# Kernel optimization log

Measured on AMD Instinct MI355X. Metric: run time of the kernel, lower is better.

## Reference

```python
import jax, jax.numpy as jnp
import numpy as np

N = 32768      # total points (multiple of patch_size -> no padding needed)
C = 768        # channels
H = 8          # num heads
K = 256        # patch_size (window length)
HD = C // H    # head dim = 96, divisible by 6 (3 axes * rotary pairs)
FREQ = 100.0   # rope_freq


def rope3d(x, pos):
    """Point-position RoPE: head dim split into 3 axis chunks, each rotated
    by angles pos_axis * freq**(-i/half).  x: [N,H,HD], pos: [N,3] float."""
    d_axis = HD // 3            # 32
    half = d_axis // 2          # 16
    inv_freq = FREQ ** (-jnp.arange(half, dtype=x.dtype) / half)   # [half]
    ang = pos[:, :, None] * inv_freq[None, None, :]                # [N,3,half]
    cos = jnp.cos(ang)[:, None, :, :]                              # [N,1,3,half]
    sin = jnp.sin(ang)[:, None, :, :]
    xr = x.reshape(x.shape[0], x.shape[1], 3, d_axis)              # [N,H,3,d_axis]
    x1, x2 = xr[..., :half], xr[..., half:]
    out = jnp.concatenate([x1 * cos - x2 * sin, x1 * sin + x2 * cos], axis=-1)
    return out.reshape(x.shape)


def setup_inputs() -> dict:
    key = jax.random.key(0)
    ks = jax.random.split(key, 6)
    feat = jax.random.normal(ks[0], (N, C), dtype=jnp.float32)
    grid_coord = jax.random.randint(ks[1], (N, 3), 0, 1024, dtype=jnp.int32)
    order = jax.random.permutation(ks[2], N).astype(jnp.int32)     # serialized order
    inverse = jnp.argsort(order).astype(jnp.int32)                 # its inverse
    w_qkv = jax.random.normal(ks[3], (C, 3 * C), dtype=jnp.float32) * 0.02
    b_qkv = jnp.zeros((3 * C,), dtype=jnp.float32)
    w_proj = jax.random.normal(ks[4], (C, C), dtype=jnp.float32) * 0.02
    b_proj = jnp.zeros((C,), dtype=jnp.float32)
    return {"feat": feat, "grid_coord": grid_coord, "order": order,
            "inverse": inverse, "w_qkv": w_qkv, "b_qkv": b_qkv,
            "w_proj": w_proj, "b_proj": b_proj}


def reference(feat, grid_coord, order, inverse, w_qkv, b_qkv, w_proj, b_proj):
    scale = HD ** -0.5
    P = N // K  # number of windows
    qkv = (feat @ w_qkv + b_qkv)[order]                   # gather by serialized order
    pos = grid_coord[order].astype(feat.dtype)            # [N,3]
    q, k, v = jnp.split(qkv, 3, axis=-1)
    q = rope3d(q.reshape(N, H, HD), pos)
    k = rope3d(k.reshape(N, H, HD), pos)
    v = v.reshape(N, H, HD)
    # windowed (varlen with equal patch lengths) attention
    qw = q.reshape(P, K, H, HD)
    kw = k.reshape(P, K, H, HD)
    vw = v.reshape(P, K, H, HD)
    logits = jnp.einsum('pqhd,pkhd->phqk', qw, kw) * scale
    attn = jax.nn.softmax(logits, axis=-1)
    out = jnp.einsum('phqk,pkhd->pqhd', attn, vw).reshape(N, C)
    out = out[inverse]                                    # scatter back to input order
    return out @ w_proj + b_proj
```

## Files before the change

### kernel.cpp

```cpp
#include <hip/hip_runtime.h>
#include <hip/hip_bf16.h>
#include <stdint.h>

typedef __bf16 bf16_t;
typedef __bf16 bf16x8 __attribute__((ext_vector_type(8)));
typedef __bf16 bf16x4 __attribute__((ext_vector_type(4)));
typedef float f32x4 __attribute__((ext_vector_type(4)));

__device__ __forceinline__ void gload_lds16(const bf16_t* g, bf16_t* l) {
  __builtin_amdgcn_global_load_lds((const __attribute__((address_space(1))) void*)g,
                                   (__attribute__((address_space(3))) void*)l, 16, 0, 0);
}

__global__ __launch_bounds__(256) void transpose_cast_k(const float* __restrict__ W,
                                                        bf16_t* __restrict__ Bt,
                                                        int KDin, int MDin) {
  __shared__ float tile[64][65];
  const int bm = blockIdx.x, bk = blockIdx.y;
  const int c = threadIdx.x & 63, r0 = threadIdx.x >> 6;
#pragma unroll
  for (int rr = 0; rr < 16; ++rr) {
    int row = rr * 4 + r0;
    tile[row][c] = W[(size_t)(bk * 64 + row) * MDin + bm * 64 + c];
  }
  __syncthreads();
#pragma unroll
  for (int rr = 0; rr < 16; ++rr) {
    int mo = rr * 4 + r0;
    Bt[(size_t)(bm * 64 + mo) * KDin + bk * 64 + c] = (bf16_t)tile[c][mo];
  }
}

__global__ __launch_bounds__(256) void gather_cast_k(const float* __restrict__ feat,
                                                     const int* __restrict__ order,
                                                     const int* __restrict__ grid_coord,
                                                     bf16_t* __restrict__ featp,
                                                     float* __restrict__ posf) {
  const int id = blockIdx.x * 256 + threadIdx.x;
  const int j = id / 192;
  const int c = (id % 192) * 4;
  const int g = order[j];
  const float4 v = *(const float4*)(feat + (size_t)g * 768 + c);
  bf16x4 o;
  o[0] = (bf16_t)v.x; o[1] = (bf16_t)v.y; o[2] = (bf16_t)v.z; o[3] = (bf16_t)v.w;
  *(bf16x4*)(featp + (size_t)j * 768 + c) = o;
  if (c == 0) {
    posf[j * 3 + 0] = (float)grid_coord[g * 3 + 0];
    posf[j * 3 + 1] = (float)grid_coord[g * 3 + 1];
    posf[j * 3 + 2] = (float)grid_coord[g * 3 + 2];
  }
}

template <int MODE>
__global__ __launch_bounds__(256) void gemm_bt_k(const bf16_t* __restrict__ A,
                                                 const bf16_t* __restrict__ Bt,
                                                 const float* __restrict__ bias,
                                                 bf16_t* __restrict__ Cq,
                                                 bf16_t* __restrict__ Ck,
                                                 bf16_t* __restrict__ Cv,
                                                 float* __restrict__ Cf,
                                                 const int* __restrict__ order,
                                                 const float* __restrict__ posf) {
  __shared__ bf16_t As[128 * 32];
  __shared__ bf16_t Bs[128 * 32];
  const int tid = threadIdx.x;
  const int lane = tid & 63;
  const int wave = tid >> 6;
  const int wr = wave >> 1, wc = wave & 1;
  const int lq = lane & 15, lk = lane >> 4;
  const int bx = blockIdx.x, by = blockIdx.y;

  const bf16_t* gA = A + (size_t)(by * 128 + (tid >> 2)) * 768 + (tid & 3) * 8;
  const bf16_t* gB = Bt + (size_t)(bx * 128 + (tid >> 2)) * 768 + (tid & 3) * 8;
  bf16_t* lA = As + tid * 8;
  bf16_t* lB = Bs + tid * 8;

  f32x4 acc[4][4] = {};

  for (int kk = 0; kk < 24; ++kk) {
    gload_lds16(gA, lA);
    gload_lds16(gA + 64 * 768, lA + 2048);
    gload_lds16(gB, lB);
    gload_lds16(gB + 64 * 768, lB + 2048);
    gA += 32;
    gB += 32;
    __syncthreads();
    bf16x8 af[4], bfr[4];
#pragma unroll
    for (int t = 0; t < 4; ++t) {
      af[t]  = *(const bf16x8*)(As + (wr * 64 + t * 16 + lq) * 32 + lk * 8);
      bfr[t] = *(const bf16x8*)(Bs + (wc * 64 + t * 16 + lq) * 32 + lk * 8);
    }
#pragma unroll
    for (int mt = 0; mt < 4; ++mt)
#pragma unroll
      for (int nt = 0; nt < 4; ++nt)
        acc[mt][nt] = __builtin_amdgcn_mfma_f32_16x16x32_bf16(af[mt], bfr[nt], acc[mt][nt], 0, 0, 0);
    __syncthreads();
  }

  const int colb = bx * 128 + wc * 64;
  float bcol[4];
#pragma unroll
  for (int nt = 0; nt < 4; ++nt) bcol[nt] = bias[colb + nt * 16 + lq];

  if (MODE == 0) {
    bf16_t* base = (bx < 6) ? Cq : (bx < 12 ? Ck : Cv);
    const int coll = colb - (bx < 6 ? 0 : (bx < 12 ? 768 : 1536));
    if (bx < 12) {
      const int a0 = (colb % 96) >> 5;
      const int a1 = ((colb + 32) % 96) >> 5;
      const float fr = exp2f(-0.41524101186f * (float)lq);
#pragma unroll
      for (int mt = 0; mt < 4; ++mt) {
        const int rowb = by * 128 + wr * 64 + mt * 16 + lk * 4;
#pragma unroll
        for (int r = 0; r < 4; ++r) {
          const int row = rowb + r;
          float s0, c0, s1, c1;
          __sincosf(posf[row * 3 + a0] * fr, &s0, &c0);
          __sincosf(posf[row * 3 + a1] * fr, &s1, &c1);
          const float x1 = acc[mt][0][r] + bcol[0], x2 = acc[mt][1][r] + bcol[1];
          const float y1 = acc[mt][2][r] + bcol[2], y2 = acc[mt][3][r] + bcol[3];
          acc[mt][0][r] = x1 * c0 - x2 * s0;
          acc[mt][1][r] = x1 * s0 + x2 * c0;
          acc[mt][2][r] = y1 * c1 - y2 * s1;
          acc[mt][3][r] = y1 * s1 + y2 * c1;
        }
#pragma unroll
        for (int nt = 0; nt < 4; ++nt) {
          const int col = coll + nt * 16 + lq;
#pragma unroll
          for (int r = 0; r < 4; ++r)
            base[(size_t)(rowb + r) * 768 + col] = (bf16_t)acc[mt][nt][r];
        }
      }
    } else {
#pragma unroll
      for (int mt = 0; mt < 4; ++mt) {
        const int rowb = by * 128 + wr * 64 + mt * 16 + lk * 4;
#pragma unroll
        for (int nt = 0; nt < 4; ++nt) {
          const int col = coll + nt * 16 + lq;
#pragma unroll
          for (int r = 0; r < 4; ++r)
            base[(size_t)(rowb + r) * 768 + col] = (bf16_t)(acc[mt][nt][r] + bcol[nt]);
        }
      }
    }
  } else {
#pragma unroll
    for (int mt = 0; mt < 4; ++mt) {
      const int rowb = by * 128 + wr * 64 + mt * 16 + lk * 4;
      int ro[4];
#pragma unroll
      for (int r = 0; r < 4; ++r) ro[r] = order[rowb + r];
#pragma unroll
      for (int nt = 0; nt < 4; ++nt) {
        const int col = colb + nt * 16 + lq;
#pragma unroll
        for (int r = 0; r < 4; ++r)
          Cf[(size_t)ro[r] * 768 + col] = acc[mt][nt][r] + bcol[nt];
      }
    }
  }
}

__global__ __launch_bounds__(256) void pack_k(const bf16_t* __restrict__ Kb,
                                              const bf16_t* __restrict__ Vb,
                                              bf16_t* __restrict__ Kp,
                                              bf16_t* __restrict__ Vp) {
  __shared__ bf16_t VT[96 * 264];
  const int h = blockIdx.x, p = blockIdx.y;
  const int tid = threadIdx.x;
  const int tok0 = p * 256;
  const size_t phb = (size_t)(p * 8 + h) * 24576;

#pragma unroll
  for (int i = 0; i < 12; ++i) {
    const int c = i * 256 + tid;
    const int fi = c >> 6, ln = c & 63;
    const int nt = fi / 3, a = fi - nt * 3;
    const int tok = nt * 16 + (ln & 15), feat = a * 32 + (ln >> 4) * 8;
    *(bf16x8*)(Kp + phb + (size_t)c * 8) =
        *(const bf16x8*)(Kb + (size_t)(tok0 + tok) * 768 + h * 96 + feat);
  }

  {
    const bf16_t* vrow = Vb + (size_t)(tok0 + tid) * 768 + h * 96;
#pragma unroll
    for (int d0 = 0; d0 < 96; d0 += 8) {
      bf16x8 v = *(const bf16x8*)(vrow + d0);
#pragma unroll
      for (int i = 0; i < 8; ++i) VT[(d0 + i) * 264 + tid] = v[i];
    }
  }
  __syncthreads();
#pragma unroll
  for (int i = 0; i < 12; ++i) {
    const int c = i * 256 + tid;
    const int fi = c >> 6, ln = c & 63;
    const int d = (fi >> 3) * 16 + (ln & 15);
    const int tb = (fi & 7) * 32 + (ln >> 4) * 8;
    *(bf16x8*)(Vp + phb + (size_t)c * 8) = *(const bf16x8*)(VT + d * 264 + tb);
  }
}

__global__ __launch_bounds__(256) void attn_k(bf16_t* QO,
                                              const bf16_t* __restrict__ Kp,
                                              const bf16_t* __restrict__ Vp) {
  __shared__ bf16_t KV[24576];
  __shared__ bf16_t Pb[4][2048];
  const int bid = blockIdx.x;
  const int chunk = bid & 3;
  const int ph = bid >> 2;
  const int h = ph & 7, p = ph >> 3;
  const int tid = threadIdx.x, lane = tid & 63, wave = tid >> 6;
  const int lq = lane & 15, lk = lane >> 4;
  const int tok0 = p * 256;
  const int qrow0 = chunk * 64 + wave * 16;
  const bf16_t* Kps = Kp + (size_t)ph * 24576;
  const bf16_t* Vps = Vp + (size_t)ph * 24576;
  const float scale = 0.10206207262f;

#pragma unroll
  for (int i = 0; i < 12; ++i)
    gload_lds16(Kps + i * 2048 + tid * 8, KV + i * 2048 + tid * 8);
  bf16x8 aq[3];
  {
    const bf16_t* qb = QO + (size_t)(tok0 + qrow0 + lq) * 768 + h * 96 + lk * 8;
#pragma unroll
    for (int kc = 0; kc < 3; ++kc) aq[kc] = *(const bf16x8*)(qb + kc * 32);
  }
  __syncthreads();

  f32x4 sacc[16];
#pragma unroll
  for (int nt = 0; nt < 16; ++nt) {
    f32x4 acc = {0.f, 0.f, 0.f, 0.f};
#pragma unroll
    for (int kc = 0; kc < 3; ++kc) {
      bf16x8 bk = *(const bf16x8*)(KV + (size_t)((nt * 3 + kc) * 64 + lane) * 8);
      acc = __builtin_amdgcn_mfma_f32_16x16x32_bf16(aq[kc], bk, acc, 0, 0, 0);
    }
    sacc[nt] = acc;
  }
  __syncthreads();

#pragma unroll
  for (int i = 0; i < 12; ++i)
    gload_lds16(Vps + i * 2048 + tid * 8, KV + i * 2048 + tid * 8);

  float linv[4];
#pragma unroll
  for (int r = 0; r < 4; ++r) {
    float mx = -1e30f;
#pragma unroll
    for (int nt = 0; nt < 16; ++nt) mx = fmaxf(mx, sacc[nt][r]);
    mx = fmaxf(mx, __shfl_xor(mx, 1));
    mx = fmaxf(mx, __shfl_xor(mx, 2));
    mx = fmaxf(mx, __shfl_xor(mx, 4));
    mx = fmaxf(mx, __shfl_xor(mx, 8));
    mx *= scale;
    float l = 0.f;
#pragma unroll
    for (int nt = 0; nt < 16; ++nt) {
      float e = __expf(sacc[nt][r] * scale - mx);
      sacc[nt][r] = e;
      l += e;
    }
    l += __shfl_xor(l, 1);
    l += __shfl_xor(l, 2);
    l += __shfl_xor(l, 4);
    l += __shfl_xor(l, 8);
    linv[r] = 1.f / l;
  }
  __syncthreads();

  bf16_t* pw = &Pb[wave][0];
  f32x4 oacc[6] = {};
#pragma unroll
  for (int hf = 0; hf < 2; ++hf) {
#pragma unroll
    for (int ntl = 0; ntl < 8; ++ntl) {
      const int nt = hf * 8 + ntl;
      const int chk = ntl * 2 + (lq >> 3);
#pragma unroll
      for (int r = 0; r < 4; ++r) {
        const int row = lk * 4 + r;
        const int phys = chk ^ (row & 7);
        pw[row * 128 + phys * 8 + (lq & 7)] = (bf16_t)sacc[nt][r];
      }
    }
#pragma unroll
    for (int kcl = 0; kcl < 4; ++kcl) {
      const int physr = (kcl * 4 + lk) ^ (lq & 7);
      bf16x8 pf = *(const bf16x8*)(pw + lq * 128 + physr * 8);
      const int kc = hf * 4 + kcl;
#pragma unroll
      for (int dt = 0; dt < 6; ++dt) {
        bf16x8 vb = *(const bf16x8*)(KV + (size_t)((dt * 8 + kc) * 64 + lane) * 8);
        oacc[dt] = __builtin_amdgcn_mfma_f32_16x16x32_bf16(pf, vb, oacc[dt], 0, 0, 0);
      }
    }
  }

#pragma unroll
  for (int dt = 0; dt < 6; ++dt) {
#pragma unroll
    for (int r = 0; r < 4; ++r) {
      const int row = tok0 + qrow0 + lk * 4 + r;
      QO[(size_t)row * 768 + h * 96 + dt * 16 + lq] = (bf16_t)(oacc[dt][r] * linv[r]);
    }
  }
}

extern "C" void kernel_launch(void* const* d_in, const int* in_sizes, int n_in,
                              void* d_out, int out_size, void* d_ws, size_t ws_size,
                              hipStream_t stream) {
  const float* feat       = (const float*)d_in[0];
  const int*   grid_coord = (const int*)d_in[1];
  const int*   order      = (const int*)d_in[2];
  const float* w_qkv      = (const float*)d_in[4];
  const float* b_qkv      = (const float*)d_in[5];
  const float* w_proj     = (const float*)d_in[6];
  const float* b_proj     = (const float*)d_in[7];
  float* out = (float*)d_out;

  char* ws = (char*)d_ws;
  bf16_t* Bt1   = (bf16_t*)(ws);
  bf16_t* Bt2   = (bf16_t*)(ws + 3538944);
  bf16_t* featp = (bf16_t*)(ws + 4718592);
  bf16_t* Kp    = featp;
  bf16_t* Qb    = (bf16_t*)(ws + 55050240);
  bf16_t* Kb    = (bf16_t*)(ws + 105381888);
  bf16_t* Vb    = (bf16_t*)(ws + 155713536);
  bf16_t* Vp    = (bf16_t*)(ws + 206045184);
  float*  posf  = (float*)(ws + 206045184);

  transpose_cast_k<<<dim3(36, 12), 256, 0, stream>>>(w_qkv, Bt1, 768, 2304);
  transpose_cast_k<<<dim3(12, 12), 256, 0, stream>>>(w_proj, Bt2, 768, 768);
  gather_cast_k<<<24576, 256, 0, stream>>>(feat, order, grid_coord, featp, posf);
  gemm_bt_k<0><<<dim3(18, 256), 256, 0, stream>>>(featp, Bt1, b_qkv, Qb, Kb, Vb, nullptr, nullptr, posf);
  pack_k<<<dim3(8, 128), 256, 0, stream>>>(Kb, Vb, Kp, Vp);
  attn_k<<<4096, 256, 0, stream>>>(Qb, Kp, Vp);
  gemm_bt_k<1><<<dim3(6, 256), 256, 0, stream>>>(Qb, Bt2, b_proj, nullptr, nullptr, nullptr, out, order, nullptr);
}
```

Measured before the change: 528.5 us.

## Replace GEMMs with 256x256-tile, 4-stage pipelined, swizzled-LDS kernel

The 128x128 single-buffered GEMM is replaced by a 512-thread 256x256-tile kernel. It keeps a four-deep ring of LDS stages filled with direct global-to-LDS loads, waits on explicit vmcnt counts, and raises wave priority around the MFMA blocks. It also XOR-swizzles the LDS slots to avoid bank conflicts and remaps block IDs so neighbouring blocks share tiles. The aim is to hide global-load latency behind MFMA work and raise reuse per loaded byte. In exchange it needs 128KB of dynamic LDS and many accumulator registers, and gives fewer blocks for the projection GEMM (384).

Result: faster. 502.8 us (-4.9%).

```diff
diff --git a/kernel.cpp b/kernel.cpp
--- a/kernel.cpp
+++ b/kernel.cpp
@@ -6,6 +6,8 @@
 typedef __bf16 bf16x8 __attribute__((ext_vector_type(8)));
 typedef __bf16 bf16x4 __attribute__((ext_vector_type(4)));
 typedef float f32x4 __attribute__((ext_vector_type(4)));
+
+template <int V> struct ic { static constexpr int value = V; };
 
 __device__ __forceinline__ void gload_lds16(const bf16_t* g, bf16_t* l) {
   __builtin_amdgcn_global_load_lds((const __attribute__((address_space(1))) void*)g,
@@ -51,116 +53,169 @@
   }
 }
 
-template <int MODE>
-__global__ __launch_bounds__(256) void gemm_bt_k(const bf16_t* __restrict__ A,
-                                                 const bf16_t* __restrict__ Bt,
-                                                 const float* __restrict__ bias,
-                                                 bf16_t* __restrict__ Cq,
-                                                 bf16_t* __restrict__ Ck,
-                                                 bf16_t* __restrict__ Cv,
-                                                 float* __restrict__ Cf,
-                                                 const int* __restrict__ order,
-                                                 const float* __restrict__ posf) {
-  __shared__ bf16_t As[128 * 32];
-  __shared__ bf16_t Bs[128 * 32];
+template <int MODE, int NBX>
+__global__ __launch_bounds__(512, 2) void gemm256_k(const bf16_t* __restrict__ A,
+                                                    const bf16_t* __restrict__ Bt,
+                                                    const float* __restrict__ bias,
+                                                    bf16_t* __restrict__ Cq,
+                                                    bf16_t* __restrict__ Ck,
+                                                    bf16_t* __restrict__ Cv,
+                                                    float* __restrict__ Cf,
+                                                    const int* __restrict__ order,
+                                                    const float* __restrict__ posf) {
+  extern __shared__ bf16_t sm[];
+  bf16_t* ldsA = sm;
+  bf16_t* ldsB = sm + 4 * 8192;
+
   const int tid = threadIdx.x;
-  const int lane = tid & 63;
-  const int wave = tid >> 6;
-  const int wr = wave >> 1, wc = wave & 1;
+  const int lane = tid & 63, wave = tid >> 6;
+  const int wr = wave >> 2, wc = wave & 3;
   const int lq = lane & 15, lk = lane >> 4;
-  const int bx = blockIdx.x, by = blockIdx.y;
-
-  const bf16_t* gA = A + (size_t)(by * 128 + (tid >> 2)) * 768 + (tid & 3) * 8;
-  const bf16_t* gB = Bt + (size_t)(bx * 128 + (tid >> 2)) * 768 + (tid & 3) * 8;
-  bf16_t* lA = As + tid * 8;
-  bf16_t* lB = Bs + tid * 8;
-
-  f32x4 acc[4][4] = {};
-
-  for (int kk = 0; kk < 24; ++kk) {
-    gload_lds16(gA, lA);
-    gload_lds16(gA + 64 * 768, lA + 2048);
-    gload_lds16(gB, lB);
-    gload_lds16(gB + 64 * 768, lB + 2048);
-    gA += 32;
-    gB += 32;
-    __syncthreads();
+
+  const int bid = blockIdx.x;
+  const int cpx = gridDim.x >> 3;
+  const int rm = (bid & 7) * cpx + (bid >> 3);
+  const int by = rm / NBX, bx = rm % NBX;
+
+  const int o0 = tid, o1 = tid + 512;
+  const int r0s = o0 >> 2, ls0 = (o0 & 3) ^ ((r0s >> 1) & 3);
+  const int r1s = o1 >> 2, ls1 = (o1 & 3) ^ ((r1s >> 1) & 3);
+  const bf16_t* pA0 = A + (size_t)(by * 256 + r0s) * 768 + ls0 * 8;
+  const bf16_t* pA1 = A + (size_t)(by * 256 + r1s) * 768 + ls1 * 8;
+  const bf16_t* pB0 = Bt + (size_t)(bx * 256 + r0s) * 768 + ls0 * 8;
+  const bf16_t* pB1 = Bt + (size_t)(bx * 256 + r1s) * 768 + ls1 * 8;
+
+  auto stageA = [&](int kt) {
+    bf16_t* d = ldsA + ((kt & 3) << 13);
+    gload_lds16(pA0 + kt * 32, d + o0 * 8);
+    gload_lds16(pA1 + kt * 32, d + o1 * 8);
+  };
+  auto stageB = [&](int kt) {
+    bf16_t* d = ldsB + ((kt & 3) << 13);
+    gload_lds16(pB0 + kt * 32, d + o0 * 8);
+    gload_lds16(pB1 + kt * 32, d + o1 * 8);
+  };
+
+  const int pslot = lk ^ ((lq >> 1) & 3);
+
+  f32x4 acc[8][4] = {};
+
+  stageA(0); stageB(0); stageA(1); stageB(1); stageA(2); stageB(2);
+  asm volatile("s_waitcnt vmcnt(8)" ::: "memory");
+  __builtin_amdgcn_s_barrier();
+  __builtin_amdgcn_sched_barrier(0);
+
+  auto group = [&](int t, auto VMC, auto STGC) {
+    constexpr int VM = decltype(VMC)::value;
+    constexpr bool STG = decltype(STGC)::value;
+    const bf16_t* Ab = ldsA + ((t & 3) << 13);
+    const bf16_t* Bb = ldsB + ((t & 3) << 13);
     bf16x8 af[4], bfr[4];
 #pragma unroll
-    for (int t = 0; t < 4; ++t) {
-      af[t]  = *(const bf16x8*)(As + (wr * 64 + t * 16 + lq) * 32 + lk * 8);
-      bfr[t] = *(const bf16x8*)(Bs + (wc * 64 + t * 16 + lq) * 32 + lk * 8);
-    }
-#pragma unroll
-    for (int mt = 0; mt < 4; ++mt)
-#pragma unroll
-      for (int nt = 0; nt < 4; ++nt)
-        acc[mt][nt] = __builtin_amdgcn_mfma_f32_16x16x32_bf16(af[mt], bfr[nt], acc[mt][nt], 0, 0, 0);
-    __syncthreads();
-  }
-
-  const int colb = bx * 128 + wc * 64;
+    for (int m = 0; m < 4; ++m)
+      af[m] = *(const bf16x8*)(Ab + (wr * 128 + m * 16 + lq) * 32 + pslot * 8);
+#pragma unroll
+    for (int n = 0; n < 4; ++n)
+      bfr[n] = *(const bf16x8*)(Bb + (wc * 64 + n * 16 + lq) * 32 + pslot * 8);
+    if constexpr (STG) stageA(t + 3);
+    __builtin_amdgcn_s_barrier();
+    asm volatile("s_waitcnt lgkmcnt(0)" ::: "memory");
+    __builtin_amdgcn_s_setprio(1);
+#pragma unroll
+    for (int n = 0; n < 4; ++n)
+#pragma unroll
+      for (int m = 0; m < 4; ++m)
+        acc[m][n] = __builtin_amdgcn_mfma_f32_16x16x32_bf16(af[m], bfr[n], acc[m][n], 0, 0, 0);
+    __builtin_amdgcn_s_setprio(0);
+    __builtin_amdgcn_s_barrier();
+#pragma unroll
+    for (int m = 0; m < 4; ++m)
+      af[m] = *(const bf16x8*)(Ab + (wr * 128 + 64 + m * 16 + lq) * 32 + pslot * 8);
+    if constexpr (STG) stageB(t + 3);
+    if constexpr (VM == 8) asm volatile("s_waitcnt vmcnt(8)" ::: "memory");
+    else if constexpr (VM == 4) asm volatile("s_waitcnt vmcnt(4)" ::: "memory");
+    else if constexpr (VM == 0) asm volatile("s_waitcnt vmcnt(0)" ::: "memory");
+    __builtin_amdgcn_s_barrier();
+    asm volatile("s_waitcnt lgkmcnt(0)" ::: "memory");
+    __builtin_amdgcn_s_setprio(1);
+#pragma unroll
+    for (int n = 0; n < 4; ++n)
+#pragma unroll
+      for (int m = 0; m < 4; ++m)
+        acc[4 + m][n] = __builtin_amdgcn_mfma_f32_16x16x32_bf16(af[m], bfr[n], acc[4 + m][n], 0, 0, 0);
+    __builtin_amdgcn_s_setprio(0);
+    __builtin_amdgcn_s_barrier();
+    __builtin_amdgcn_sched_barrier(0);
+  };
+
+  for (int t = 0; t < 21; ++t) group(t, ic<8>{}, ic<1>{});
+  group(21, ic<4>{}, ic<0>{});
+  group(22, ic<0>{}, ic<0>{});
+  group(23, ic<-1>{}, ic<0>{});
+
+  const int colb = bx * 256 + wc * 64;
   float bcol[4];
 #pragma unroll
-  for (int nt = 0; nt < 4; ++nt) bcol[nt] = bias[colb + nt * 16 + lq];
+  for (int n = 0; n < 4; ++n) bcol[n] = bias[colb + n * 16 + lq];
 
   if (MODE == 0) {
-    bf16_t* base = (bx < 6) ? Cq : (bx < 12 ? Ck : Cv);
-    const int coll = colb - (bx < 6 ? 0 : (bx < 12 ? 768 : 1536));
-    if (bx < 12) {
+    const int sec = bx / 3;
+    bf16_t* base = sec == 0 ? Cq : (sec == 1 ? Ck : Cv);
+    const int coll = colb - sec * 768;
+    if (sec < 2) {
       const int a0 = (colb % 96) >> 5;
       const int a1 = ((colb + 32) % 96) >> 5;
       const float fr = exp2f(-0.41524101186f * (float)lq);
 #pragma unroll
-      for (int mt = 0; mt < 4; ++mt) {
-        const int rowb = by * 128 + wr * 64 + mt * 16 + lk * 4;
+      for (int m = 0; m < 8; ++m) {
+        const int rowb = by * 256 + wr * 128 + m * 16 + lk * 4;
 #pragma unroll
         for (int r = 0; r < 4; ++r) {
           const int row = rowb + r;
           float s0, c0, s1, c1;
           __sincosf(posf[row * 3 + a0] * fr, &s0, &c0);
           __sincosf(posf[row * 3 + a1] * fr, &s1, &c1);
-          const float x1 = acc[mt][0][r] + bcol[0], x2 = acc[mt][1][r] + bcol[1];
-          const float y1 = acc[mt][2][r] + bcol[2], y2 = acc[mt][3][r] + bcol[3];
-          acc[mt][0][r] = x1 * c0 - x2 * s0;
-          acc[mt][1][r] = x1 * s0 + x2 * c0;
-          acc[mt][2][r] = y1 * c1 - y2 * s1;
-          acc[mt][3][r] = y1 * s1 + y2 * c1;
+          const float x1 = acc[m][0][r] + bcol[0], x2 = acc[m][1][r] + bcol[1];
+          const float y1 = acc[m][2][r] + bcol[2], y2 = acc[m][3][r] + bcol[3];
+          acc[m][0][r] = x1 * c0 - x2 * s0;
+          acc[m][1][r] = x1 * s0 + x2 * c0;
+          acc[m][2][r] = y1 * c1 - y2 * s1;
+          acc[m][3][r] = y1 * s1 + y2 * c1;
         }
 #pragma unroll
-        for (int nt = 0; nt < 4; ++nt) {
-          const int col = coll + nt * 16 + lq;
+        for (int n = 0; n < 4; ++n) {
+          const int col = coll + n * 16 + lq;
 #pragma unroll
           for (int r = 0; r < 4; ++r)
-            base[(size_t)(rowb + r) * 768 + col] = (bf16_t)acc[mt][nt][r];
+            base[(size_t)(rowb + r) * 768 + col] = (bf16_t)acc[m][n][r];
         }
       }
     } else {
 #pragma unroll
-      for (int mt = 0; mt < 4; ++mt) {
-        const int rowb = by * 128 + wr * 64 + mt * 16 + lk * 4;
-#pragma unroll
-        for (int nt = 0; nt < 4; ++nt) {
-          const int col = coll + nt * 16 + lq;
+      for (int m = 0; m < 8; ++m) {
+        const int rowb = by * 256 + wr * 128 + m * 16 + lk * 4;
+#pragma unroll
+        for (int n = 0; n < 4; ++n) {
+          const int col = coll + n * 16 + lq;
 #pragma unroll
           for (int r = 0; r < 4; ++r)
-            base[(size_t)(rowb + r) * 768 + col] = (bf16_t)(acc[mt][nt][r] + bcol[nt]);
+            base[(size_t)(rowb + r) * 768 + col] = (bf16_t)(acc[m][n][r] + bcol[n]);
         }
       }
     }
   } else {
 #pragma unroll
-    for (int mt = 0; mt < 4; ++mt) {
-      const int rowb = by * 128 + wr * 64 + mt * 16 + lk * 4;
+    for (int m = 0; m < 8; ++m) {
+      const int rowb = by * 256 + wr * 128 + m * 16 + lk * 4;
       int ro[4];
 #pragma unroll
       for (int r = 0; r < 4; ++r) ro[r] = order[rowb + r];
 #pragma unroll
-      for (int nt = 0; nt < 4; ++nt) {
-        const int col = colb + nt * 16 + lq;
+      for (int n = 0; n < 4; ++n) {
+        const int col = colb + n * 16 + lq;
 #pragma unroll
         for (int r = 0; r < 4; ++r)
-          Cf[(size_t)ro[r] * 768 + col] = acc[mt][nt][r] + bcol[nt];
+          Cf[(size_t)ro[r] * 768 + col] = acc[m][n][r] + bcol[n];
       }
     }
   }
@@ -338,11 +393,22 @@
   bf16_t* Vp    = (bf16_t*)(ws + 206045184);
   float*  posf  = (float*)(ws + 206045184);
 
+  static bool attr_set = false;
+  if (!attr_set) {
+    (void)hipFuncSetAttribute((const void*)gemm256_k<0, 9>,
+                              hipFuncAttributeMaxDynamicSharedMemorySize, 131072);
+    (void)hipFuncSetAttribute((const void*)gemm256_k<1, 3>,
+                              hipFuncAttributeMaxDynamicSharedMemorySize, 131072);
+    attr_set = true;
+  }
+
   transpose_cast_k<<<dim3(36, 12), 256, 0, stream>>>(w_qkv, Bt1, 768, 2304);
   transpose_cast_k<<<dim3(12, 12), 256, 0, stream>>>(w_proj, Bt2, 768, 768);
   gather_cast_k<<<24576, 256, 0, stream>>>(feat, order, grid_coord, featp, posf);
-  gemm_bt_k<0><<<dim3(18, 256), 256, 0, stream>>>(featp, Bt1, b_qkv, Qb, Kb, Vb, nullptr, nullptr, posf);
+  gemm256_k<0, 9><<<1152, 512, 131072, stream>>>(featp, Bt1, b_qkv, Qb, Kb, Vb,
+                                                 nullptr, nullptr, posf);
   pack_k<<<dim3(8, 128), 256, 0, stream>>>(Kb, Vb, Kp, Vp);
   attn_k<<<4096, 256, 0, stream>>>(Qb, Kp, Vp);
-  gemm_bt_k<1><<<dim3(6, 256), 256, 0, stream>>>(Qb, Bt2, b_proj, nullptr, nullptr, nullptr, out, order, nullptr);
-}
+  gemm256_k<1, 3><<<384, 512, 131072, stream>>>(Qb, Bt2, b_proj, nullptr, nullptr,
+                                                nullptr, out, order, nullptr);
+}
```
